# Performance work log

Hardware: AMD Instinct MI355X
Metric: run time of the kernel (lower is better)

Reference implementation:

```python
import jax, jax.numpy as jnp
import numpy as np

N = 20000
E = 320000
IN_FEAT = 256
HID = 256
OUT_FEAT = 128


def setup_inputs() -> dict:
    key = jax.random.key(0)
    ks = jax.random.split(key, 10)
    inp = {
        "x": jax.random.normal(ks[0], (N, IN_FEAT), dtype=jnp.float32),
        "edge_src": jax.random.randint(ks[1], (E,), 0, N, dtype=jnp.int32),
        "edge_dst": jax.random.randint(ks[2], (E,), 0, N, dtype=jnp.int32),
        "edge_w": jax.random.uniform(ks[3], (E,), dtype=jnp.float32),
        # params (Linear weights stored as [out, in], torch convention)
        "W_emb": jax.random.normal(ks[4], (HID, IN_FEAT), dtype=jnp.float32) / np.sqrt(IN_FEAT),
        "W_gc1": jax.random.normal(ks[5], (HID, 2 * HID), dtype=jnp.float32) / np.sqrt(2 * HID),
        "b_gc1": jnp.zeros((HID,), dtype=jnp.float32),
        "W_gc2": jax.random.normal(ks[6], (HID, 2 * HID), dtype=jnp.float32) / np.sqrt(2 * HID),
        "b_gc2": jnp.zeros((HID,), dtype=jnp.float32),
        "W_fc": jax.random.normal(ks[7], (OUT_FEAT, HID), dtype=jnp.float32) / np.sqrt(HID),
    }
    return inp


def reference(x, edge_src, edge_dst, edge_w, W_emb, W_gc1, b_gc1, W_gc2, b_gc2, W_fc):
    n = x.shape[0]

    def adj_mul(h):
        msgs = h[edge_src] * edge_w[:, None]           # [E, hid]
        return jax.ops.segment_sum(msgs, edge_dst, num_segments=n)

    def gconv(h, W, b):
        cat = jnp.concatenate([h, adj_mul(h)], axis=1)  # [N, 2*hid]
        return cat @ W.T + b

    h = x @ W_emb.T                                    # embedding (no bias)
    h = h + jax.nn.relu(gconv(h, W_gc1, b_gc1))        # residual (dropout = eval identity)
    h = h + jax.nn.relu(gconv(h, W_gc2, b_gc2))
    out = h @ W_fc.T                                   # fc_last (no bias)
    out = out / jnp.sqrt(jnp.sum(out * out, axis=1, keepdims=True))
    return out
```

## Files before the change

kernel.cpp:

```cpp
#include <hip/hip_runtime.h>
#include <math.h>

#define N_NODES 20000
#define E_EDGES 320000
#define HID 256
#define OUT_FEAT 128
#define MPAD 20224
#define CAP 64

#define BK 64
#define LSTR 72

typedef __attribute__((ext_vector_type(8))) __bf16 bf16x8;
typedef __attribute__((ext_vector_type(4))) float floatx4;


#define WBLK 176
#define EBLK 1250

__global__ void convert_scatter_kernel(
    const float* __restrict__ w0, const float* __restrict__ w1,
    const float* __restrict__ w2, const float* __restrict__ w3,
    __bf16* __restrict__ o0, __bf16* __restrict__ o1,
    __bf16* __restrict__ o2, __bf16* __restrict__ o3,
    const int* __restrict__ src, const int* __restrict__ dst,
    const float* __restrict__ w, int* __restrict__ counts,
    int2* __restrict__ edges) {
    const int b = blockIdx.x;
    if (b < WBLK) {
        const size_t gi = ((size_t)b * 256 + threadIdx.x) * 8;
        const size_t s0 = 65536, s1 = s0 + 131072, s2 = s1 + 131072, s3 = s2 + 32768;
        if (gi >= s3) return;
        const float* srcp; __bf16* dstp; size_t off;
        if (gi < s0)      { srcp = w0; dstp = o0; off = gi; }
        else if (gi < s1) { srcp = w1; dstp = o1; off = gi - s0; }
        else if (gi < s2) { srcp = w2; dstp = o2; off = gi - s1; }
        else              { srcp = w3; dstp = o3; off = gi - s2; }
        float4 v0 = *(const float4*)(srcp + off);
        float4 v1 = *(const float4*)(srcp + off + 4);
        bf16x8 o;
        o[0] = (__bf16)v0.x; o[1] = (__bf16)v0.y; o[2] = (__bf16)v0.z; o[3] = (__bf16)v0.w;
        o[4] = (__bf16)v1.x; o[5] = (__bf16)v1.y; o[6] = (__bf16)v1.z; o[7] = (__bf16)v1.w;
        *(bf16x8*)(dstp + off) = o;
    } else {
        int e = (b - WBLK) * 256 + threadIdx.x;
        if (e < E_EDGES) {
            int d = dst[e];
            int p = atomicAdd(&counts[d], 1);
            edges[(size_t)d * CAP + p] = make_int2(src[e], __float_as_int(w[e]));
        }
    }
}


__global__ __launch_bounds__(256) void aggregate_kernel(
    const __bf16* __restrict__ h, const int* __restrict__ counts,
    const int2* __restrict__ edges, __bf16* __restrict__ agg) {
    const int w = threadIdx.x >> 6, lane = threadIdx.x & 63;
    const int half = lane >> 5, lh = lane & 31;
    const int d = blockIdx.x * 8 + w * 2 + half;
    const size_t base = (size_t)d * CAP;
    const int iters = (counts[d] + 15) >> 4;
    float acc[8];
#pragma unroll
    for (int q = 0; q < 8; q++) acc[q] = 0.f;

    for (int it = 0; it < iters; ++it) {
        const int2* ep = edges + base + it * 16;
        int4 eh[8];
#pragma unroll
        for (int u = 0; u < 8; u++) eh[u] = *(const int4*)(ep + u * 2);
        bf16x8 hv[16];
#pragma unroll
        for (int u = 0; u < 8; u++) {
            hv[u * 2]     = *(const bf16x8*)(h + (size_t)eh[u].x * HID + lh * 8);
            hv[u * 2 + 1] = *(const bf16x8*)(h + (size_t)eh[u].z * HID + lh * 8);
        }
#pragma unroll
        for (int u = 0; u < 8; u++) {
            float wa = __int_as_float(eh[u].y), wb = __int_as_float(eh[u].w);
#pragma unroll
            for (int q = 0; q < 8; q++) {
                acc[q] = fmaf(wa, (float)hv[u * 2][q], acc[q]);
                acc[q] = fmaf(wb, (float)hv[u * 2 + 1][q], acc[q]);
            }
        }
    }
    bf16x8 o;
#pragma unroll
    for (int q = 0; q < 8; q++) o[q] = (__bf16)acc[q];
    *(bf16x8*)(agg + (size_t)d * HID + lh * 8) = o;
}


template <int KTOT, int EPI, bool F32A>
__global__ __launch_bounds__(256) void gemm64_kernel(
    const __bf16* __restrict__ A1,
    const float* __restrict__ A1f,
    const __bf16* __restrict__ A2,
    const __bf16* __restrict__ W,
    const float* __restrict__ bias,
    const __bf16* __restrict__ hres,
    __bf16* __restrict__ outb)
{
    __shared__ __bf16 As[64 * LSTR];
    __shared__ __bf16 Bs[128 * LSTR];
    const int tid = threadIdx.x;
    const int row0 = blockIdx.y * 64;
    const int col0 = blockIdx.x * 128;
    const int wv = tid >> 6, l = tid & 63, lr = l & 15, lq = l >> 4;
    const int wm = wv & 1, wn = wv >> 1;

    floatx4 acc[2][4];
#pragma unroll
    for (int i = 0; i < 2; i++)
#pragma unroll
        for (int j = 0; j < 4; j++) acc[i][j] = (floatx4){0.f, 0.f, 0.f, 0.f};

    const int srow = tid >> 3;
    const int skq = (tid & 7) * 8;

    for (int kc = 0; kc < KTOT; kc += BK) {
        if (F32A) {
#pragma unroll
            for (int r = 0; r < 2; r++) {
                int row = r * 32 + srow;
                int grow = row0 + row;
                float4 v0 = make_float4(0.f, 0.f, 0.f, 0.f), v1 = v0;
                if (grow < N_NODES) {
                    const float* xp = A1f + (size_t)grow * HID + kc + skq;
                    v0 = *(const float4*)xp;
                    v1 = *(const float4*)(xp + 4);
                }
                bf16x8 o;
                o[0] = (__bf16)v0.x; o[1] = (__bf16)v0.y; o[2] = (__bf16)v0.z; o[3] = (__bf16)v0.w;
                o[4] = (__bf16)v1.x; o[5] = (__bf16)v1.y; o[6] = (__bf16)v1.z; o[7] = (__bf16)v1.w;
                *(bf16x8*)&As[row * LSTR + skq] = o;
            }
        } else {
            const __bf16* Asrc = (KTOT == 512 && kc >= 256) ? A2 : A1;
            const int ks = (KTOT == 512) ? (kc & 255) : kc;
#pragma unroll
            for (int r = 0; r < 2; r++) {
                int row = r * 32 + srow;
                *(bf16x8*)&As[row * LSTR + skq] =
                    *(const bf16x8*)(Asrc + (size_t)(row0 + row) * HID + ks + skq);
            }
        }
#pragma unroll
        for (int r = 0; r < 4; r++) {
            int row = r * 32 + srow;
            *(bf16x8*)&Bs[row * LSTR + skq] =
                *(const bf16x8*)(W + (size_t)(col0 + row) * KTOT + kc + skq);
        }
        __syncthreads();
#pragma unroll
        for (int s = 0; s < 2; s++) {
            bf16x8 af[2], bfr[4];
#pragma unroll
            for (int mt = 0; mt < 2; mt++)
                af[mt] = *(const bf16x8*)&As[(wm * 32 + mt * 16 + lr) * LSTR + s * 32 + lq * 8];
#pragma unroll
            for (int nt = 0; nt < 4; nt++)
                bfr[nt] = *(const bf16x8*)&Bs[(wn * 64 + nt * 16 + lr) * LSTR + s * 32 + lq * 8];
#pragma unroll
            for (int mt = 0; mt < 2; mt++)
#pragma unroll
                for (int nt = 0; nt < 4; nt++)
                    acc[mt][nt] = __builtin_amdgcn_mfma_f32_16x16x32_bf16(af[mt], bfr[nt], acc[mt][nt], 0, 0, 0);
        }
        __syncthreads();
    }

#pragma unroll
    for (int nt = 0; nt < 4; nt++) {
        const int col = col0 + wn * 64 + nt * 16 + lr;
        float b = 0.f;
        if (EPI == 1) b = bias[col];
#pragma unroll
        for (int mt = 0; mt < 2; mt++) {
            const int row = row0 + wm * 32 + mt * 16 + lq * 4;
#pragma unroll
            for (int r = 0; r < 4; r++) {
                float v = acc[mt][nt][r];
                if (EPI == 1) {
                    float res = (float)hres[(size_t)(row + r) * HID + col];
                    v = res + fmaxf(v + b, 0.f);
                }
                outb[(size_t)(row + r) * HID + col] = (__bf16)v;
            }
        }
    }
}


#define TSTR 264

__global__ __launch_bounds__(512) void gconv_fc_kernel(
    const __bf16* __restrict__ hp,
    const __bf16* __restrict__ ag,
    const __bf16* __restrict__ W,
    const float* __restrict__ bias,
    const __bf16* __restrict__ Wfc,
    float* __restrict__ outp)
{
    __shared__ __bf16 smem[64 * LSTR + 256 * LSTR];
    __bf16* As = smem;
    __bf16* Bs = smem + 64 * LSTR;
    const int tid = threadIdx.x;
    const int row0 = blockIdx.x * 64;
    const int wv = tid >> 6, l = tid & 63, lr = l & 15, lq = l >> 4;
    const int wm = wv & 1, wn4 = wv >> 1;

    floatx4 acc[2][4];
#pragma unroll
    for (int i = 0; i < 2; i++)
#pragma unroll
        for (int j = 0; j < 4; j++) acc[i][j] = (floatx4){0.f, 0.f, 0.f, 0.f};

    const int srow = tid >> 3;
    const int skq = (tid & 7) * 8;

    for (int kc = 0; kc < 512; kc += BK) {
        const __bf16* Asrc = (kc >= 256) ? ag : hp;
        const int ks = kc & 255;
        *(bf16x8*)&As[srow * LSTR + skq] =
            *(const bf16x8*)(Asrc + (size_t)(row0 + srow) * HID + ks + skq);
#pragma unroll
        for (int r = 0; r < 4; r++) {
            int row = r * 64 + srow;
            *(bf16x8*)&Bs[row * LSTR + skq] =
                *(const bf16x8*)(W + (size_t)row * 512 + kc + skq);
        }
        __syncthreads();
#pragma unroll
        for (int s = 0; s < 2; s++) {
            bf16x8 af[2], bfr[4];
#pragma unroll
            for (int mt = 0; mt < 2; mt++)
                af[mt] = *(const bf16x8*)&As[(wm * 32 + mt * 16 + lr) * LSTR + s * 32 + lq * 8];
#pragma unroll
            for (int nt = 0; nt < 4; nt++)
                bfr[nt] = *(const bf16x8*)&Bs[(wn4 * 64 + nt * 16 + lr) * LSTR + s * 32 + lq * 8];
#pragma unroll
            for (int mt = 0; mt < 2; mt++)
#pragma unroll
                for (int nt = 0; nt < 4; nt++)
                    acc[mt][nt] = __builtin_amdgcn_mfma_f32_16x16x32_bf16(af[mt], bfr[nt], acc[mt][nt], 0, 0, 0);
        }
        __syncthreads();
    }

    __bf16 (*tile)[TSTR] = (__bf16(*)[TSTR])smem;
#pragma unroll
    for (int nt = 0; nt < 4; nt++) {
        const int col = wn4 * 64 + nt * 16 + lr;
        const float b = bias[col];
#pragma unroll
        for (int mt = 0; mt < 2; mt++) {
            const int lrow = wm * 32 + mt * 16 + lq * 4;
#pragma unroll
            for (int r = 0; r < 4; r++) {
                float res = (float)hp[(size_t)(row0 + lrow + r) * HID + col];
                float v = res + fmaxf(acc[mt][nt][r] + b, 0.f);
                tile[lrow + r][col] = (__bf16)v;
            }
        }
    }
    __syncthreads();

    if (wv < 4) {
        floatx4 facc[8];
#pragma unroll
        for (int j = 0; j < 8; j++) facc[j] = (floatx4){0.f, 0.f, 0.f, 0.f};
#pragma unroll
        for (int kt = 0; kt < 256; kt += 32) {
            bf16x8 a = *(const bf16x8*)&tile[wv * 16 + lr][kt + lq * 8];
            bf16x8 bf8[8];
#pragma unroll
            for (int nt = 0; nt < 8; nt++)
                bf8[nt] = *(const bf16x8*)(Wfc + (size_t)(nt * 16 + lr) * 256 + kt + lq * 8);
#pragma unroll
            for (int nt = 0; nt < 8; nt++)
                facc[nt] = __builtin_amdgcn_mfma_f32_16x16x32_bf16(a, bf8[nt], facc[nt], 0, 0, 0);
        }
        float s[4];
#pragma unroll
        for (int r = 0; r < 4; r++) {
            float t = 0.f;
#pragma unroll
            for (int nt = 0; nt < 8; nt++) t = fmaf(facc[nt][r], facc[nt][r], t);
            s[r] = t;
        }
#pragma unroll
        for (int mask = 1; mask <= 8; mask <<= 1) {
#pragma unroll
            for (int r = 0; r < 4; r++) s[r] += __shfl_xor(s[r], mask);
        }
        float inv[4];
#pragma unroll
        for (int r = 0; r < 4; r++) inv[r] = rsqrtf(s[r]);
#pragma unroll
        for (int r = 0; r < 4; r++) {
            int row = row0 + wv * 16 + lq * 4 + r;
            if (row >= N_NODES) continue;
#pragma unroll
            for (int nt = 0; nt < 8; nt++)
                outp[(size_t)row * OUT_FEAT + nt * 16 + lr] = facc[nt][r] * inv[r];
        }
    }
}


extern "C" void kernel_launch(void* const* d_in, const int* in_sizes, int n_in,
                              void* d_out, int out_size, void* d_ws, size_t ws_size,
                              hipStream_t stream) {
    const float* x        = (const float*)d_in[0];
    const int*   edge_src = (const int*)d_in[1];
    const int*   edge_dst = (const int*)d_in[2];
    const float* edge_w   = (const float*)d_in[3];
    const float* W_emb    = (const float*)d_in[4];
    const float* W_gc1    = (const float*)d_in[5];
    const float* b_gc1    = (const float*)d_in[6];
    const float* W_gc2    = (const float*)d_in[7];
    const float* b_gc2    = (const float*)d_in[8];
    const float* W_fc     = (const float*)d_in[9];
    float* out = (float*)d_out;

    char* p = (char*)d_ws;
    const size_t HROW = (size_t)MPAD * HID;
    __bf16* hb0   = (__bf16*)p;             p += HROW * 2;
    __bf16* hb1   = (__bf16*)p;             p += HROW * 2;
    __bf16* aggb  = (__bf16*)p;             p += HROW * 2;
    __bf16* wemb  = (__bf16*)p;             p += 65536 * 2;
    __bf16* w1b   = (__bf16*)p;             p += 131072 * 2;
    __bf16* w2b   = (__bf16*)p;             p += 131072 * 2;
    __bf16* wfcb  = (__bf16*)p;             p += 32768 * 2;
    int2*   edges = (int2*)p;               p += (size_t)N_NODES * CAP * 8;
    int*    counts = (int*)p;               p += (size_t)MPAD * 4;

    hipMemsetAsync(counts, 0, (size_t)MPAD * 4, stream);
    hipMemsetAsync(edges, 0, (size_t)N_NODES * CAP * 8, stream);

    convert_scatter_kernel<<<WBLK + EBLK, 256, 0, stream>>>(
        W_emb, W_gc1, W_gc2, W_fc, wemb, w1b, w2b, wfcb,
        edge_src, edge_dst, edge_w, counts, edges);

    const dim3 grid_g(2, MPAD / 64);

    gemm64_kernel<256, 0, true><<<grid_g, 256, 0, stream>>>(
        nullptr, x, nullptr, wemb, nullptr, nullptr, hb0);
    aggregate_kernel<<<N_NODES / 8, 256, 0, stream>>>(hb0, counts, edges, aggb);
    gemm64_kernel<512, 1, false><<<grid_g, 256, 0, stream>>>(
        hb0, nullptr, aggb, w1b, b_gc1, hb0, hb1);
    aggregate_kernel<<<N_NODES / 8, 256, 0, stream>>>(hb1, counts, edges, aggb);
    gconv_fc_kernel<<<MPAD / 64, 512, 0, stream>>>(hb1, aggb, w2b, b_gc2, wfcb, out);
}
```

Measured before the change: 203.6 us.

## Fuse embedding GEMM with edge scatter and weight conversion; drop edges memset

Merges the weight-conversion/edge-scatter kernel and the embedding GEMM into one front kernel. Block ranges do the x@W_emb GEMM (converting W_emb to bf16 on the fly), the edge bucketing, or the conversion of the remaining weights, which removes one launch and the separate W_emb conversion. The large memset that zeroed the edge buckets is removed. Aggregation now masks out-of-count slots, sending them to row 0 with weight 0, so unwritten bucket entries are safe. The risk is that the mixed-role kernel has imbalanced blocks, and the scatter blocks no longer bounds-check e (EBLK*256 equals E exactly).

```diff
diff --git a/kernel.cpp b/kernel.cpp
--- a/kernel.cpp
+++ b/kernel.cpp
@@ -15,40 +15,116 @@
 typedef __attribute__((ext_vector_type(4))) float floatx4;
 
 
-#define WBLK 176
-#define EBLK 1250
-
-__global__ void convert_scatter_kernel(
-    const float* __restrict__ w0, const float* __restrict__ w1,
-    const float* __restrict__ w2, const float* __restrict__ w3,
-    __bf16* __restrict__ o0, __bf16* __restrict__ o1,
-    __bf16* __restrict__ o2, __bf16* __restrict__ o3,
+#define EMB_BLK 632
+#define SCAT_BLK 1250
+#define CONV_BLK 144
+
+__global__ __launch_bounds__(256) void front_kernel(
+    const float* __restrict__ x,
+    const float* __restrict__ wembf,
+    __bf16* __restrict__ hb0,
     const int* __restrict__ src, const int* __restrict__ dst,
     const float* __restrict__ w, int* __restrict__ counts,
-    int2* __restrict__ edges) {
-    const int b = blockIdx.x;
-    if (b < WBLK) {
-        const size_t gi = ((size_t)b * 256 + threadIdx.x) * 8;
-        const size_t s0 = 65536, s1 = s0 + 131072, s2 = s1 + 131072, s3 = s2 + 32768;
-        if (gi >= s3) return;
+    int2* __restrict__ edges,
+    const float* __restrict__ w1f, const float* __restrict__ w2f,
+    const float* __restrict__ wfcf,
+    __bf16* __restrict__ w1b, __bf16* __restrict__ w2b,
+    __bf16* __restrict__ wfcb)
+{
+    __shared__ __bf16 As[64 * LSTR];
+    __shared__ __bf16 Bs[128 * LSTR];
+    const int bid = blockIdx.x;
+    const int tid = threadIdx.x;
+
+    if (bid < EMB_BLK) {
+        const int row0 = (bid >> 1) * 64;
+        const int col0 = (bid & 1) * 128;
+        const int wv = tid >> 6, l = tid & 63, lr = l & 15, lq = l >> 4;
+        const int wm = wv & 1, wn = wv >> 1;
+
+        floatx4 acc[2][4];
+#pragma unroll
+        for (int i = 0; i < 2; i++)
+#pragma unroll
+            for (int j = 0; j < 4; j++) acc[i][j] = (floatx4){0.f, 0.f, 0.f, 0.f};
+
+        const int srow = tid >> 3;
+        const int skq = (tid & 7) * 8;
+
+        for (int kc = 0; kc < 256; kc += BK) {
+#pragma unroll
+            for (int r = 0; r < 2; r++) {
+                int row = r * 32 + srow;
+                int grow = row0 + row;
+                float4 v0 = make_float4(0.f, 0.f, 0.f, 0.f), v1 = v0;
+                if (grow < N_NODES) {
+                    const float* xp = x + (size_t)grow * HID + kc + skq;
+                    v0 = *(const float4*)xp;
+                    v1 = *(const float4*)(xp + 4);
+                }
+                bf16x8 o;
+                o[0] = (__bf16)v0.x; o[1] = (__bf16)v0.y; o[2] = (__bf16)v0.z; o[3] = (__bf16)v0.w;
+                o[4] = (__bf16)v1.x; o[5] = (__bf16)v1.y; o[6] = (__bf16)v1.z; o[7] = (__bf16)v1.w;
+                *(bf16x8*)&As[row * LSTR + skq] = o;
+            }
+#pragma unroll
+            for (int r = 0; r < 4; r++) {
+                int row = r * 32 + srow;
+                const float* wp = wembf + (size_t)(col0 + row) * 256 + kc + skq;
+                float4 v0 = *(const float4*)wp;
+                float4 v1 = *(const float4*)(wp + 4);
+                bf16x8 o;
+                o[0] = (__bf16)v0.x; o[1] = (__bf16)v0.y; o[2] = (__bf16)v0.z; o[3] = (__bf16)v0.w;
+                o[4] = (__bf16)v1.x; o[5] = (__bf16)v1.y; o[6] = (__bf16)v1.z; o[7] = (__bf16)v1.w;
+                *(bf16x8*)&Bs[row * LSTR + skq] = o;
+            }
+            __syncthreads();
+#pragma unroll
+            for (int s = 0; s < 2; s++) {
+                bf16x8 af[2], bfr[4];
+#pragma unroll
+                for (int mt = 0; mt < 2; mt++)
+                    af[mt] = *(const bf16x8*)&As[(wm * 32 + mt * 16 + lr) * LSTR + s * 32 + lq * 8];
+#pragma unroll
+                for (int nt = 0; nt < 4; nt++)
+                    bfr[nt] = *(const bf16x8*)&Bs[(wn * 64 + nt * 16 + lr) * LSTR + s * 32 + lq * 8];
+#pragma unroll
+                for (int mt = 0; mt < 2; mt++)
+#pragma unroll
+                    for (int nt = 0; nt < 4; nt++)
+                        acc[mt][nt] = __builtin_amdgcn_mfma_f32_16x16x32_bf16(af[mt], bfr[nt], acc[mt][nt], 0, 0, 0);
+            }
+            __syncthreads();
+        }
+#pragma unroll
+        for (int nt = 0; nt < 4; nt++) {
+            const int col = col0 + wn * 64 + nt * 16 + lr;
+#pragma unroll
+            for (int mt = 0; mt < 2; mt++) {
+                const int row = row0 + wm * 32 + mt * 16 + lq * 4;
+#pragma unroll
+                for (int r = 0; r < 4; r++)
+                    hb0[(size_t)(row + r) * HID + col] = (__bf16)acc[mt][nt][r];
+            }
+        }
+    } else if (bid < EMB_BLK + SCAT_BLK) {
+        int e = (bid - EMB_BLK) * 256 + tid;
+        int d = dst[e];
+        int p = atomicAdd(&counts[d], 1);
+        edges[(size_t)d * CAP + p] = make_int2(src[e], __float_as_int(w[e]));
+    } else {
+        const size_t gi = ((size_t)(bid - EMB_BLK - SCAT_BLK) * 256 + tid) * 8;
+        const size_t s1 = 131072, s2 = 262144;
         const float* srcp; __bf16* dstp; size_t off;
-        if (gi < s0)      { srcp = w0; dstp = o0; off = gi; }
-        else if (gi < s1) { srcp = w1; dstp = o1; off = gi - s0; }
-        else if (gi < s2) { srcp = w2; dstp = o2; off = gi - s1; }
-        else              { srcp = w3; dstp = o3; off = gi - s2; }
+        if (gi < s1)      { srcp = w1f; dstp = w1b; off = gi; }
+        else if (gi < s2) { srcp = w2f; dstp = w2b; off = gi - s1; }
+        else              { srcp = wfcf; dstp = wfcb; off = gi - s2; }
         float4 v0 = *(const float4*)(srcp + off);
         float4 v1 = *(const float4*)(srcp + off + 4);
         bf16x8 o;
         o[0] = (__bf16)v0.x; o[1] = (__bf16)v0.y; o[2] = (__bf16)v0.z; o[3] = (__bf16)v0.w;
         o[4] = (__bf16)v1.x; o[5] = (__bf16)v1.y; o[6] = (__bf16)v1.z; o[7] = (__bf16)v1.w;
         *(bf16x8*)(dstp + off) = o;
-    } else {
-        int e = (b - WBLK) * 256 + threadIdx.x;
-        if (e < E_EDGES) {
-            int d = dst[e];
-            int p = atomicAdd(&counts[d], 1);
-            edges[(size_t)d * CAP + p] = make_int2(src[e], __float_as_int(w[e]));
-        }
     }
 }
 
@@ -60,30 +136,37 @@
     const int half = lane >> 5, lh = lane & 31;
     const int d = blockIdx.x * 8 + w * 2 + half;
     const size_t base = (size_t)d * CAP;
-    const int iters = (counts[d] + 15) >> 4;
+    const int cnt = counts[d];
+    const int iters = (cnt + 15) >> 4;
     float acc[8];
 #pragma unroll
     for (int q = 0; q < 8; q++) acc[q] = 0.f;
 
     for (int it = 0; it < iters; ++it) {
-        const int2* ep = edges + base + it * 16;
+        const int jb = it * 16;
+        const int2* ep = edges + base + jb;
         int4 eh[8];
 #pragma unroll
         for (int u = 0; u < 8; u++) eh[u] = *(const int4*)(ep + u * 2);
+        int sidx[16]; float wv[16];
+#pragma unroll
+        for (int u = 0; u < 8; u++) {
+            const bool m0 = (jb + u * 2)     < cnt;
+            const bool m1 = (jb + u * 2 + 1) < cnt;
+            sidx[u * 2]     = m0 ? eh[u].x : 0;
+            wv[u * 2]       = m0 ? __int_as_float(eh[u].y) : 0.f;
+            sidx[u * 2 + 1] = m1 ? eh[u].z : 0;
+            wv[u * 2 + 1]   = m1 ? __int_as_float(eh[u].w) : 0.f;
+        }
         bf16x8 hv[16];
 #pragma unroll
-        for (int u = 0; u < 8; u++) {
-            hv[u * 2]     = *(const bf16x8*)(h + (size_t)eh[u].x * HID + lh * 8);
-            hv[u * 2 + 1] = *(const bf16x8*)(h + (size_t)eh[u].z * HID + lh * 8);
-        }
-#pragma unroll
-        for (int u = 0; u < 8; u++) {
-            float wa = __int_as_float(eh[u].y), wb = __int_as_float(eh[u].w);
-#pragma unroll
-            for (int q = 0; q < 8; q++) {
-                acc[q] = fmaf(wa, (float)hv[u * 2][q], acc[q]);
-                acc[q] = fmaf(wb, (float)hv[u * 2 + 1][q], acc[q]);
-            }
+        for (int u = 0; u < 16; u++)
+            hv[u] = *(const bf16x8*)(h + (size_t)sidx[u] * HID + lh * 8);
+#pragma unroll
+        for (int u = 0; u < 16; u++) {
+#pragma unroll
+            for (int q = 0; q < 8; q++)
+                acc[q] = fmaf(wv[u], (float)hv[u][q], acc[q]);
         }
     }
     bf16x8 o;
@@ -93,15 +176,12 @@
 }
 
 
-template <int KTOT, int EPI, bool F32A>
-__global__ __launch_bounds__(256) void gemm64_kernel(
-    const __bf16* __restrict__ A1,
-    const float* __restrict__ A1f,
-    const __bf16* __restrict__ A2,
+__global__ __launch_bounds__(256) void gconv1_kernel(
+    const __bf16* __restrict__ hp,
+    const __bf16* __restrict__ ag,
     const __bf16* __restrict__ W,
     const float* __restrict__ bias,
-    const __bf16* __restrict__ hres,
-    __bf16* __restrict__ outb)
+    __bf16* __restrict__ hn)
 {
     __shared__ __bf16 As[64 * LSTR];
     __shared__ __bf16 Bs[128 * LSTR];
@@ -120,38 +200,20 @@
     const int srow = tid >> 3;
     const int skq = (tid & 7) * 8;
 
-    for (int kc = 0; kc < KTOT; kc += BK) {
-        if (F32A) {
-#pragma unroll
-            for (int r = 0; r < 2; r++) {
-                int row = r * 32 + srow;
-                int grow = row0 + row;
-                float4 v0 = make_float4(0.f, 0.f, 0.f, 0.f), v1 = v0;
-                if (grow < N_NODES) {
-                    const float* xp = A1f + (size_t)grow * HID + kc + skq;
-                    v0 = *(const float4*)xp;
-                    v1 = *(const float4*)(xp + 4);
-                }
-                bf16x8 o;
-                o[0] = (__bf16)v0.x; o[1] = (__bf16)v0.y; o[2] = (__bf16)v0.z; o[3] = (__bf16)v0.w;
-                o[4] = (__bf16)v1.x; o[5] = (__bf16)v1.y; o[6] = (__bf16)v1.z; o[7] = (__bf16)v1.w;
-                *(bf16x8*)&As[row * LSTR + skq] = o;
-            }
-        } else {
-            const __bf16* Asrc = (KTOT == 512 && kc >= 256) ? A2 : A1;
-            const int ks = (KTOT == 512) ? (kc & 255) : kc;
-#pragma unroll
-            for (int r = 0; r < 2; r++) {
-                int row = r * 32 + srow;
-                *(bf16x8*)&As[row * LSTR + skq] =
-                    *(const bf16x8*)(Asrc + (size_t)(row0 + row) * HID + ks + skq);
-            }
+    for (int kc = 0; kc < 512; kc += BK) {
+        const __bf16* Asrc = (kc >= 256) ? ag : hp;
+        const int ks = kc & 255;
+#pragma unroll
+        for (int r = 0; r < 2; r++) {
+            int row = r * 32 + srow;
+            *(bf16x8*)&As[row * LSTR + skq] =
+                *(const bf16x8*)(Asrc + (size_t)(row0 + row) * HID + ks + skq);
         }
 #pragma unroll
         for (int r = 0; r < 4; r++) {
             int row = r * 32 + srow;
             *(bf16x8*)&Bs[row * LSTR + skq] =
-                *(const bf16x8*)(W + (size_t)(col0 + row) * KTOT + kc + skq);
+                *(const bf16x8*)(W + (size_t)(col0 + row) * 512 + kc + skq);
         }
         __syncthreads();
 #pragma unroll
@@ -175,19 +237,15 @@
 #pragma unroll
     for (int nt = 0; nt < 4; nt++) {
         const int col = col0 + wn * 64 + nt * 16 + lr;
-        float b = 0.f;
-        if (EPI == 1) b = bias[col];
+        const float b = bias[col];
 #pragma unroll
         for (int mt = 0; mt < 2; mt++) {
             const int row = row0 + wm * 32 + mt * 16 + lq * 4;
 #pragma unroll
             for (int r = 0; r < 4; r++) {
-                float v = acc[mt][nt][r];
-                if (EPI == 1) {
-                    float res = (float)hres[(size_t)(row + r) * HID + col];
-                    v = res + fmaxf(v + b, 0.f);
-                }
-                outb[(size_t)(row + r) * HID + col] = (__bf16)v;
+                float res = (float)hp[(size_t)(row + r) * HID + col];
+                float v = res + fmaxf(acc[mt][nt][r] + b, 0.f);
+                hn[(size_t)(row + r) * HID + col] = (__bf16)v;
             }
         }
     }
@@ -332,7 +390,6 @@
     __bf16* hb0   = (__bf16*)p;             p += HROW * 2;
     __bf16* hb1   = (__bf16*)p;             p += HROW * 2;
     __bf16* aggb  = (__bf16*)p;             p += HROW * 2;
-    __bf16* wemb  = (__bf16*)p;             p += 65536 * 2;
     __bf16* w1b   = (__bf16*)p;             p += 131072 * 2;
     __bf16* w2b   = (__bf16*)p;             p += 131072 * 2;
     __bf16* wfcb  = (__bf16*)p;             p += 32768 * 2;
@@ -340,19 +397,16 @@
     int*    counts = (int*)p;               p += (size_t)MPAD * 4;
 
     hipMemsetAsync(counts, 0, (size_t)MPAD * 4, stream);
-    hipMemsetAsync(edges, 0, (size_t)N_NODES * CAP * 8, stream);
-
-    convert_scatter_kernel<<<WBLK + EBLK, 256, 0, stream>>>(
-        W_emb, W_gc1, W_gc2, W_fc, wemb, w1b, w2b, wfcb,
-        edge_src, edge_dst, edge_w, counts, edges);
-
-    const dim3 grid_g(2, MPAD / 64);
-
-    gemm64_kernel<256, 0, true><<<grid_g, 256, 0, stream>>>(
-        nullptr, x, nullptr, wemb, nullptr, nullptr, hb0);
+
+    front_kernel<<<EMB_BLK + SCAT_BLK + CONV_BLK, 256, 0, stream>>>(
+        x, W_emb, hb0, edge_src, edge_dst, edge_w, counts, edges,
+        W_gc1, W_gc2, W_fc, w1b, w2b, wfcb);
+
     aggregate_kernel<<<N_NODES / 8, 256, 0, stream>>>(hb0, counts, edges, aggb);
-    gemm64_kernel<512, 1, false><<<grid_g, 256, 0, stream>>>(
-        hb0, nullptr, aggb, w1b, b_gc1, hb0, hb1);
+
+    gconv1_kernel<<<dim3(2, MPAD / 64), 256, 0, stream>>>(hb0, aggb, w1b, b_gc1, hb1);
+
     aggregate_kernel<<<N_NODES / 8, 256, 0, stream>>>(hb1, counts, edges, aggb);
+
     gconv_fc_kernel<<<MPAD / 64, 512, 0, stream>>>(hb1, aggb, w2b, b_gc2, wfcb, out);
 }
```

Result: no change. 202.9 us (-0.4%).
